# Optimization experiments

Measured on AMD Instinct MI355X. Metric: run time of the kernel, lower is better.

The kernel has to match this reference:

```python
import jax, jax.numpy as jnp
import numpy as np

N = 51200      # num nodes
E = 614400     # num edges
G = 256        # num graphs
T = 8          # num target capsules (GCNConv heads)
D = 128        # in_channels == out_channels
ROUTES = 3     # num_routes
BN_EPS = 1e-5


def squash(s):
    # s: (..., D). v = |s|^2/(1+|s|^2) * s/|s|
    s2 = jnp.sum(s * s, axis=-1, keepdims=True)
    return (s2 / (1.0 + s2)) * s * jax.lax.rsqrt(s2 + 1e-16)


def setup_inputs() -> dict:
    key = jax.random.key(0)
    k0, k1, k2, k3 = jax.random.split(key, 4)
    x = jax.random.normal(k0, (N, D), dtype=jnp.float32)
    edge_index = jax.random.randint(k1, (2, E), 0, N, dtype=jnp.int32)
    batch = jnp.sort(jax.random.randint(k2, (N,), 0, G, dtype=jnp.int32))
    edge_weight = jnp.ones((E,), dtype=jnp.float32)
    gamma = jnp.ones((D,), dtype=jnp.float32)
    beta = jnp.zeros((D,), dtype=jnp.float32)
    W = jax.random.normal(k3, (T, D, D), dtype=jnp.float32) * (1.0 / np.sqrt(D))
    bias = jnp.zeros((T, D), dtype=jnp.float32)
    return {"x": x, "edge_weight": edge_weight, "gamma": gamma, "beta": beta,
            "W": W, "bias": bias, "edge_index": edge_index, "batch": batch}


def reference(x, edge_weight, gamma, beta, W, bias, edge_index, batch):
    n = x.shape[0]
    row, col = edge_index[0], edge_index[1]

    # BatchNorm1d (training-mode batch stats)
    mu = jnp.mean(x, axis=0)
    var = jnp.var(x, axis=0)
    x = (x - mu) * jax.lax.rsqrt(var + BN_EPS) * gamma + beta

    # --- GCNConv per target capsule (PyG gcn_norm with self-loops) ---
    sl = jnp.arange(n, dtype=row.dtype)
    row_sl = jnp.concatenate([row, sl])
    col_sl = jnp.concatenate([col, sl])
    w_sl = jnp.concatenate([edge_weight, jnp.ones((n,), x.dtype)])
    deg = jax.ops.segment_sum(w_sl, col_sl, num_segments=n)
    dis = jnp.where(deg > 0, jax.lax.rsqrt(jnp.maximum(deg, 1e-12)), 0.0)
    norm = dis[row_sl] * w_sl * dis[col_sl]          # (E+N,)

    xW = jnp.einsum('nd,tdo->nto', x, W)             # (N, T, D)
    caps = []
    for t in range(T):  # small fixed loop over capsule heads keeps edge msgs at (E+N, D)
        msg = norm[:, None] * xW[row_sl, t]          # (E+N, D)
        caps.append(jax.ops.segment_sum(msg, col_sl, num_segments=n) + bias[t])
    u_hat = jnp.stack(caps, axis=1)                  # (N, T, D)

    # --- dynamic routing ---
    node_deg = jax.ops.segment_sum(edge_weight, row, num_segments=n)  # original edges, no self loops
    b = jnp.broadcast_to(node_deg[:, None, None], (n, T, 1))
    u_det = jax.lax.stop_gradient(u_hat)
    for _ in range(ROUTES - 1):
        c = jax.nn.softmax(b, axis=1)                               # (N, T, 1)
        s = jax.ops.segment_sum(c * u_det, batch, num_segments=G)   # (G, T, D)
        v = squash(s)[batch]                                        # (N, T, D)
        b = b + jnp.sum(u_det * v, axis=-1, keepdims=True)

    c = jax.nn.softmax(b, axis=1)
    s = jax.ops.segment_sum(c * u_hat, batch, num_segments=G)        # (G, T, D)
    cnt = jax.ops.segment_sum(jnp.ones((n,), x.dtype), batch, num_segments=G)
    x_mean = jax.ops.segment_sum(x, batch, num_segments=G) / jnp.maximum(cnt, 1.0)[:, None]
    s = s + x_mean[:, None, :]
    v = squash(s)
    # final_layer=True: per-capsule L2 norm -> (G, T)
    return jnp.sqrt(jnp.sum(v * v, axis=-1) + 1e-16)
```

## Files before the change

kernel.cpp:

```cpp
#include <hip/hip_runtime.h>
#include <hip/hip_bf16.h>
#include <math.h>

#define N_NODES 51200
#define N_EDGES 614400
#define N_GRAPHS 256
#define T_CAPS 8
#define D_DIM 128
#define BN_EPS 1e-5f
#define RCAP 256
#define NBUCK 200
#define BCAP 4096
#define EPB 1024
#define SBLK 600

typedef __attribute__((ext_vector_type(8))) __bf16 bf16x8;
typedef __attribute__((ext_vector_type(8))) unsigned short ushort8;
typedef __attribute__((ext_vector_type(4))) float f32x4;

__device__ inline f32x4 mfma16(uint4 a, uint4 b, f32x4 c) {
  return __builtin_amdgcn_mfma_f32_16x16x32_bf16(
      __builtin_bit_cast(bf16x8, a), __builtin_bit_cast(bf16x8, b), c, 0, 0, 0);
}
__device__ inline f32x4 mfma16v(uint4 a, ushort8 b, f32x4 c) {
  return __builtin_amdgcn_mfma_f32_16x16x32_bf16(
      __builtin_bit_cast(bf16x8, a), __builtin_bit_cast(bf16x8, b), c, 0, 0, 0);
}

__device__ inline float waveReduceSum(float v) {
#pragma unroll
  for (int off = 1; off < 64; off <<= 1) v += __shfl_xor(v, off, 64);
  return v;
}
__device__ inline float bf_lo(unsigned u) { return __uint_as_float(u << 16); }
__device__ inline float bf_hi(unsigned u) { return __uint_as_float(u & 0xffff0000u); }
__device__ inline unsigned bfbits(float f) {
  unsigned u = __float_as_uint(f);
  return (u + 0x7FFFu + ((u >> 16) & 1u)) >> 16;
}

__global__ void __launch_bounds__(256) prep(const int* __restrict__ batch,
                                            const float* __restrict__ W,
                                            int* __restrict__ start, int* __restrict__ bcur,
                                            unsigned* __restrict__ Wp,
                                            unsigned* __restrict__ WTp,
                                            float* __restrict__ rawzero) {
  int i = blockIdx.x * 256 + threadIdx.x;
  if (i < NBUCK) bcur[i] = 0;
  for (int j = i; j < 2 * N_GRAPHS * D_DIM; j += N_NODES) rawzero[j] = 0.f;
  int bn = batch[i];
  if (i == 0) {
    for (int g = 0; g <= bn; g++) start[g] = 0;
  } else {
    int bp = batch[i - 1];
    for (int g = bp + 1; g <= bn; g++) start[g] = i;
  }
  if (i == N_NODES - 1)
    for (int g = bn + 1; g <= N_GRAPHS; g++) start[g] = N_NODES;
  for (int j = i; j < 65536; j += N_NODES) {
    int t = j >> 13, r = j & 8191;
    int k = r >> 7, o = r & 127;
    float a = W[(t << 14) + (k << 8) + o];
    float b = W[(t << 14) + (k << 8) + 128 + o];
    Wp[j] = bfbits(a) | (bfbits(b) << 16);
    float2 w2 = ((const float2*)W)[(t << 13) + (o << 6) + k];
    WTp[j] = bfbits(w2.x) | (bfbits(w2.y) << 16);
  }
}

__global__ void __launch_bounds__(256) scatter_x(
    const int* __restrict__ row, const int* __restrict__ col, const float* __restrict__ ew,
    int* __restrict__ bcur, uint2* __restrict__ ebuck, const float* __restrict__ x,
    const int* __restrict__ start, float* __restrict__ rawxsum, float* __restrict__ rawxsq) {
  int bid = blockIdx.x, tid = threadIdx.x;
  if (bid < SBLK) {
    __shared__ uint2 staged[EPB];
    __shared__ int hcnt[256], lbase[256], gbase[256], wpart[4];
    unsigned rx[4], ry[4];
    int bk[4], idx[4];
    int base4 = bid * 256 + tid;
    int4 c4 = ((const int4*)col)[base4];
    int4 r4 = ((const int4*)row)[base4];
    float4 w4 = ((const float4*)ew)[base4];
    rx[0] = ((unsigned)c4.x << 16) | (unsigned)r4.x; ry[0] = bfbits(w4.x); bk[0] = c4.x >> 8;
    rx[1] = ((unsigned)c4.y << 16) | (unsigned)r4.y; ry[1] = bfbits(w4.y); bk[1] = c4.y >> 8;
    rx[2] = ((unsigned)c4.z << 16) | (unsigned)r4.z; ry[2] = bfbits(w4.z); bk[2] = c4.z >> 8;
    rx[3] = ((unsigned)c4.w << 16) | (unsigned)r4.w; ry[3] = bfbits(w4.w); bk[3] = c4.w >> 8;
    hcnt[tid] = 0;
    __syncthreads();
#pragma unroll
    for (int k = 0; k < 4; k++) idx[k] = atomicAdd(&hcnt[bk[k]], 1);
    __syncthreads();
    int v = hcnt[tid];
    int lane = tid & 63, wid = tid >> 6;
    int s = v;
#pragma unroll
    for (int off = 1; off < 64; off <<= 1) {
      int t = __shfl_up(s, off, 64);
      if (lane >= off) s += t;
    }
    if (lane == 63) wpart[wid] = s;
    if (tid < NBUCK) gbase[tid] = atomicAdd(&bcur[tid], v);
    __syncthreads();
    int add = 0;
    for (int w2 = 0; w2 < wid; w2++) add += wpart[w2];
    lbase[tid] = s + add - v;
    __syncthreads();
#pragma unroll
    for (int k = 0; k < 4; k++) staged[lbase[bk[k]] + idx[k]] = make_uint2(rx[k], ry[k]);
    __syncthreads();
    for (int i = tid; i < EPB; i += 256) {
      uint2 r = staged[i];
      int b = r.x >> 24;
      int pos = gbase[b] + (i - lbase[b]);
      if (pos < BCAP) ebuck[b * BCAP + pos] = r;
    }
    return;
  }
  int b2 = bid - SBLK;
  int g = b2 >> 2, sub = b2 & 3;
  __shared__ float ls[8][128], ls2[8][128];
  int q = tid & 31, h = tid >> 5;
  int st = start[g], en = start[g + 1];
  const float4* x4 = (const float4*)x;
  float4 s = make_float4(0.f, 0.f, 0.f, 0.f), s2 = make_float4(0.f, 0.f, 0.f, 0.f);
  for (int n = st + sub * 8 + h; n < en; n += 32) {
    float4 v = x4[n * 32 + q];
    s.x += v.x; s.y += v.y; s.z += v.z; s.w += v.w;
    s2.x += v.x * v.x; s2.y += v.y * v.y; s2.z += v.z * v.z; s2.w += v.w * v.w;
  }
  *(float4*)&ls[h][4 * q] = s;
  *(float4*)&ls2[h][4 * q] = s2;
  __syncthreads();
  if (tid < 128) {
    float a = 0.f;
#pragma unroll
    for (int hh = 0; hh < 8; hh++) a += ls[hh][tid];
    atomicAdd(&rawxsum[g * D_DIM + tid], a);
  } else {
    int d = tid - 128;
    float a = 0.f;
#pragma unroll
    for (int hh = 0; hh < 8; hh++) a += ls2[hh][d];
    atomicAdd(&rawxsq[g * D_DIM + d], a);
  }
}

__global__ void __launch_bounds__(256) bn_fin(const float* __restrict__ rawxsum,
                                              const float* __restrict__ rawxsq,
                                              const float* __restrict__ gamma,
                                              const float* __restrict__ beta,
                                              float* __restrict__ scale,
                                              float* __restrict__ shift) {
  int d = blockIdx.x;
  int tid = threadIdx.x;
  __shared__ float ls[256], ls2[256];
  ls[tid] = rawxsum[tid * D_DIM + d];
  ls2[tid] = rawxsq[tid * D_DIM + d];
  __syncthreads();
  for (int off = 128; off; off >>= 1) {
    if (tid < off) {
      ls[tid] += ls[tid + off];
      ls2[tid] += ls2[tid + off];
    }
    __syncthreads();
  }
  if (tid == 0) {
    float mu = ls[0] * (1.0f / N_NODES);
    float var = ls2[0] * (1.0f / N_NODES) - mu * mu;
    float rstd = rsqrtf(var + BN_EPS);
    float sc = gamma[d] * rstd;
    scale[d] = sc;
    shift[d] = beta[d] - mu * sc;
  }
}

__global__ void __launch_bounds__(256) build(const uint2* __restrict__ ebuck,
                                             const int* __restrict__ bcur,
                                             unsigned* __restrict__ csr,
                                             int* __restrict__ nstart, int* __restrict__ ncnt,
                                             const float* __restrict__ x,
                                             const float* __restrict__ scale,
                                             const float* __restrict__ shift,
                                             float* __restrict__ dis,
                                             __hip_bfloat162* __restrict__ y) {
  int b = blockIdx.x, tid = threadIdx.x;
  __shared__ uint2 staged[BCAP];
  __shared__ unsigned outr[BCAP];
  __shared__ int hist[256], pref[256], cur[256], wpart[4];
  __shared__ float dis_l[256];
  int cnt = min(bcur[b], BCAP);
  for (int i = tid; i < cnt; i += 256) staged[i] = ebuck[b * BCAP + i];
  hist[tid] = 0;
  __syncthreads();
  for (int i = tid; i < cnt; i += 256) {
    int dl = (staged[i].x >> 16) & 255;
    atomicAdd(&hist[dl], 1);
  }
  __syncthreads();
  int v = hist[tid];
  int lane = tid & 63, wid = tid >> 6;
  int s = v;
#pragma unroll
  for (int off = 1; off < 64; off <<= 1) {
    int t = __shfl_up(s, off, 64);
    if (lane >= off) s += t;
  }
  if (lane == 63) wpart[wid] = s;
  __syncthreads();
  int add = 0;
  for (int w2 = 0; w2 < wid; w2++) add += wpart[w2];
  int p0 = s + add - v;
  pref[tid] = p0;
  cur[tid] = p0;
  __syncthreads();
  for (int i = tid; i < cnt; i += 256) {
    uint2 r = staged[i];
    int dl = (r.x >> 16) & 255;
    int p = atomicAdd(&cur[dl], 1);
    outr[p] = ((r.x & 0xFFFFu) << 16) | r.y;
  }
  __syncthreads();
  for (int i = tid; i < cnt; i += 256) csr[b * BCAP + i] = outr[i];
  int n = b * 256 + tid;
  int hc = hist[tid];
  nstart[n] = b * BCAP + p0;
  ncnt[n] = hc;
  float sw = 0.f;
  for (int j = p0; j < p0 + hc; j++) sw += bf_lo(outr[j]);
  float dv = sw + 1.0f;
  float dn = dv > 0.f ? rsqrtf(fmaxf(dv, 1e-12f)) : 0.f;
  dis[n] = dn;
  dis_l[tid] = dn;
  __syncthreads();
  const float4* x4 = (const float4*)x;
  const float4* sc4 = (const float4*)scale;
  const float4* sh4 = (const float4*)shift;
  uint2* y2 = (uint2*)y;
  for (int i = tid; i < 256 * 32; i += 256) {
    int nl = i >> 5, l = i & 31;
    float dnl = dis_l[nl];
    float4 scv = sc4[l], shv = sh4[l];
    float4 xv = x4[(b * 256 + nl) * 32 + l];
    unsigned u0 = bfbits(dnl * (xv.x * scv.x + shv.x)) |
                  (bfbits(dnl * (xv.y * scv.y + shv.y)) << 16);
    unsigned u1 = bfbits(dnl * (xv.z * scv.z + shv.z)) |
                  (bfbits(dnl * (xv.w * scv.w + shv.w)) << 16);
    y2[(b * 256 + nl) * 32 + l] = make_uint2(u0, u1);
  }
}

__global__ void __launch_bounds__(256) node_gather(const __hip_bfloat162* __restrict__ y,
                                                   const float* __restrict__ dis,
                                                   const int* __restrict__ nstart,
                                                   const int* __restrict__ ncnt,
                                                   const unsigned* __restrict__ csr,
                                                   __hip_bfloat162* __restrict__ agg) {
  int n = blockIdx.x * 4 + (threadIdx.x >> 6);
  int lane = threadIdx.x & 63;
  int st = nstart[n], c = ncnt[n];
  float2 a = __bfloat1622float2(y[n * 64 + lane]);
  int j = 0;
  for (; j + 4 <= c; j += 4) {
    unsigned r0 = csr[st + j], r1 = csr[st + j + 1], r2 = csr[st + j + 2],
             r3 = csr[st + j + 3];
    float2 v0 = __bfloat1622float2(y[(r0 >> 16) * 64 + lane]);
    float2 v1 = __bfloat1622float2(y[(r1 >> 16) * 64 + lane]);
    float2 v2 = __bfloat1622float2(y[(r2 >> 16) * 64 + lane]);
    float2 v3 = __bfloat1622float2(y[(r3 >> 16) * 64 + lane]);
    float w0 = bf_lo(r0), w1 = bf_lo(r1), w2 = bf_lo(r2), w3 = bf_lo(r3);
    a.x += w0 * v0.x + w1 * v1.x + w2 * v2.x + w3 * v3.x;
    a.y += w0 * v0.y + w1 * v1.y + w2 * v2.y + w3 * v3.y;
  }
  for (; j < c; j++) {
    unsigned r = csr[st + j];
    float2 v = __bfloat1622float2(y[(r >> 16) * 64 + lane]);
    float w = bf_lo(r);
    a.x += w * v.x;
    a.y += w * v.y;
  }
  float dn = dis[n];
  a.x *= dn;
  a.y *= dn;
  agg[n * 64 + lane] = __float22bfloat162_rn(a);
}

__global__ void __launch_bounds__(1024) routing_fused(
    const unsigned* __restrict__ agg_bf, const int* __restrict__ start,
    const unsigned* __restrict__ Wp, const unsigned* __restrict__ WTp,
    const float* __restrict__ bias, const float* __restrict__ rawxsum,
    const float* __restrict__ scale, const float* __restrict__ shift,
    float* __restrict__ out) {
  int g = blockIdx.x;
  int tid = threadIdx.x;
  int st = start[g], c = start[g + 1] - st;

  __shared__ unsigned ag_sh[RCAP * 68];
  __shared__ float dt_sh[384][T_CAPS];
  __shared__ float ac_sh[T_CAPS][D_DIM];
  __shared__ float s_sh[T_CAPS][D_DIM];
  __shared__ float wv_sh[T_CAPS][132];
  __shared__ unsigned wvpk[2][16][68];
  __shared__ unsigned short ctb[2][16][264];
  __shared__ float csum_sh[T_CAPS], bv_sh[T_CAPS], f_sh[T_CAPS], s2p[T_CAPS][2];
  __shared__ float csp_sh[32];

  float* scratch = &dt_sh[0][0];
  const uint4* aggb4 = (const uint4*)agg_bf;
  uint4* ag4 = (uint4*)ag_sh;

  for (int i = tid; i < T_CAPS * 132; i += 1024) (&wv_sh[0][0])[i] = 0.f;
  for (int i = tid; i < 2 * 16 * 68; i += 1024) (&wvpk[0][0][0])[i] = 0u;
  for (int i = tid; i < 2 * 16 * 264; i += 1024) (&ctb[0][0][0])[i] = 0;
  if (tid < T_CAPS) {
    bv_sh[tid] = 0.f;
    csum_sh[tid] = 0.125f * (float)c;
  }
  {
    int d2 = tid & 63, h = tid >> 6;
    float sx = 0.f, sy = 0.f;
    for (int n = st + h; n < st + c; n += 16) {
      unsigned u = agg_bf[n * 64 + d2];
      sx += bf_lo(u);
      sy += bf_hi(u);
    }
    scratch[h * 128 + d2 * 2] = sx;
    scratch[h * 128 + d2 * 2 + 1] = sy;
  }
  __syncthreads();
  if (tid < 128) {
    float s = 0.f;
#pragma unroll
    for (int h = 0; h < 16; h++) s += scratch[h * 128 + tid];
    s *= 0.125f;
#pragma unroll
    for (int t = 0; t < T_CAPS; t++) ac_sh[t][tid] = s;
  }
  __syncthreads();

  int tG = tid >> 7, oG = tid & 127;
  int lane = tid & 63, wv_ = tid >> 6;

  for (int iter = 0; iter < 3; iter++) {
    {
      const unsigned* Wpt = Wp + (tG << 13);
      float s = 0.f;
#pragma unroll 8
      for (int k = 0; k < 64; k++) {
        unsigned u = Wpt[(k << 7) + oG];
        s += ac_sh[tG][2 * k] * bf_lo(u) + ac_sh[tG][2 * k + 1] * bf_hi(u);
      }
      s += csum_sh[tG] * bias[(tG << 7) + oG];
      if (iter == 2) {
        float cf = (float)c;
        float ic = 1.0f / fmaxf(cf, 1.0f);
        s += (scale[oG] * rawxsum[g * D_DIM + oG] + cf * shift[oG]) * ic;
      }
      s_sh[tG][oG] = s;
      float p = waveReduceSum(s * s);
      if ((tid & 63) == 0) s2p[tG][(tid >> 6) & 1] = p;
    }
    __syncthreads();
    if (tid < T_CAPS) {
      float s2 = s2p[tid][0] + s2p[tid][1];
      float f = (s2 / (1.0f + s2)) * rsqrtf(s2 + 1e-16f);
      f_sh[tid] = f;
      if (iter == 2) out[g * T_CAPS + tid] = sqrtf(f * f * s2 + 1e-16f);
    }
    __syncthreads();
    if (iter == 2) return;
    {
      const unsigned* WTpt = WTp + (tG << 13);
      float s = 0.f;
#pragma unroll 8
      for (int k = 0; k < 64; k++) {
        unsigned u = WTpt[(k << 7) + oG];
        s += s_sh[tG][2 * k] * bf_lo(u) + s_sh[tG][2 * k + 1] * bf_hi(u);
      }
      wv_sh[tG][oG] += f_sh[tG] * s;
      float bp = bias[(tG << 7) + oG] * s_sh[tG][oG];
      bp = waveReduceSum(bp);
      if ((tid & 63) == 0) s2p[tG][(tid >> 6) & 1] = bp;
    }
    __syncthreads();
    if (tid < T_CAPS) bv_sh[tid] += f_sh[tid] * (s2p[tid][0] + s2p[tid][1]);
    __syncthreads();
    for (int i = tid; i < 512; i += 1024) {
      int t = i >> 6, kp = i & 63;
      float a = wv_sh[t][2 * kp], b = wv_sh[t][2 * kp + 1];
      unsigned ha = bfbits(a), hb = bfbits(b);
      wvpk[0][t][kp] = ha | (hb << 16);
      float ra = a - __uint_as_float(ha << 16), rb = b - __uint_as_float(hb << 16);
      wvpk[1][t][kp] = bfbits(ra) | (bfbits(rb) << 16);
    }
    if (tid < 1024) {
      (&ac_sh[0][0])[tid] = 0.f;
    }
    if (tid < T_CAPS) csum_sh[tid] = 0.f;
    __syncthreads();

    for (int cb = 0; cb < c; cb += RCAP) {
      int nv = min(RCAP, c - cb);
      int KR32 = (nv + 31) & ~31;
      int Mt = (nv + 15) >> 4;
      if (iter == 0 || c > RCAP) {
        for (int i = tid; i < nv * 16; i += 1024) {
          int r = i >> 4, k = i & 15;
          ag4[r * 17 + k] = aggb4[(size_t)(st + cb + r) * 16 + k];
        }
        for (int i = tid; i < (KR32 - nv) * 16; i += 1024) {
          int r = nv + (i >> 4), k = i & 15;
          ag4[r * 17 + k] = make_uint4(0, 0, 0, 0);
        }
        __syncthreads();
      }
      if (wv_ < Mt) {
        int q = lane >> 4, tc = lane & 15;
        int r = wv_ * 16 + tc;
        const uint4* arow = ag4 + r * 17;
        f32x4 C = {0.f, 0.f, 0.f, 0.f};
#pragma unroll
        for (int ks = 0; ks < 4; ks++) {
          uint4 A = arow[ks * 4 + q];
          uint4 Bh = *(const uint4*)&wvpk[0][tc][ks * 16 + 4 * q];
          uint4 Bl = *(const uint4*)&wvpk[1][tc][ks * 16 + 4 * q];
          C = mfma16(A, Bh, C);
          C = mfma16(A, Bl, C);
        }
        if (tc < T_CAPS) {
          float bvv = bv_sh[tc];
#pragma unroll
          for (int i2 = 0; i2 < 4; i2++) dt_sh[wv_ * 16 + 4 * q + i2][tc] = C[i2] + bvv;
        }
      }
      __syncthreads();
      if (tid < nv) {
        float l[8];
#pragma unroll
        for (int t = 0; t < 8; t++) l[t] = dt_sh[tid][t];
        float m = l[0];
#pragma unroll
        for (int t = 1; t < 8; t++) m = fmaxf(m, l[t]);
        float z = 0.f;
#pragma unroll
        for (int t = 0; t < 8; t++) {
          l[t] = __expf(l[t] - m);
          z += l[t];
        }
        float iz = 1.0f / z;
#pragma unroll
        for (int t = 0; t < 8; t++) {
          float cv = l[t] * iz;
          dt_sh[tid][t] = cv;
          unsigned hb = bfbits(cv);
          ctb[0][t][tid] = (unsigned short)hb;
          ctb[1][t][tid] = (unsigned short)bfbits(cv - __uint_as_float(hb << 16));
        }
      }
      if (c > RCAP) {
        int tail = KR32 - nv;
        for (int i = tid; i < 16 * tail; i += 1024) {
          int hh = i & 1, t = (i >> 1) & 7, n2 = nv + (i >> 4);
          ctb[hh][t][n2] = 0;
        }
      }
      __syncthreads();
      {
        int tA = tid >> 7, idx = tid & 127;
        float p = 0.f;
        for (int n = idx; n < nv; n += 128) p += dt_sh[n][tA];
        p = waveReduceSum(p);
        if (lane == 0) csp_sh[wv_] = p;
      }
      __syncthreads();
      if (tid < T_CAPS) csum_sh[tid] += csp_sh[2 * tid] + csp_sh[2 * tid + 1];
      {
        int nt = wv_ & 7, kh = wv_ >> 3;
        int tc = lane & 15, q = lane >> 4;
        f32x4 C = {0.f, 0.f, 0.f, 0.f};
        const unsigned short* agh = (const unsigned short*)ag_sh;
        int KS = KR32 >> 5;
        for (int ks = kh; ks < KS; ks += 2) {
          uint4 Ah = *(const uint4*)&ctb[0][tc][ks * 32 + 8 * q];
          uint4 Al = *(const uint4*)&ctb[1][tc][ks * 32 + 8 * q];
          int nb = ks * 32 + 8 * q, dcol = nt * 16 + tc;
          ushort8 B;
#pragma unroll
          for (int j = 0; j < 8; j++) B[j] = agh[(nb + j) * 136 + dcol];
          C = mfma16v(Ah, B, C);
          C = mfma16v(Al, B, C);
        }
        if (kh == 1) *(f32x4*)&scratch[(nt * 64 + lane) * 4] = C;
        __syncthreads();
        if (kh == 0) {
          f32x4 o4 = *(const f32x4*)&scratch[(nt * 64 + lane) * 4];
          C.x += o4.x;
          C.y += o4.y;
          C.z += o4.z;
          C.w += o4.w;
#pragma unroll
          for (int i2 = 0; i2 < 4; i2++) {
            int tt = 4 * q + i2;
            if (tt < T_CAPS) ac_sh[tt][nt * 16 + tc] += C[i2];
          }
        }
      }
      __syncthreads();
    }
  }
}

extern "C" void kernel_launch(void* const* d_in, const int* in_sizes, int n_in, void* d_out,
                              int out_size, void* d_ws, size_t ws_size, hipStream_t stream) {
  const float* x = (const float*)d_in[0];
  const float* ew = (const float*)d_in[1];
  const float* gamma = (const float*)d_in[2];
  const float* beta = (const float*)d_in[3];
  const float* W = (const float*)d_in[4];
  const float* bias = (const float*)d_in[5];
  const int* eidx = (const int*)d_in[6];
  const int* batch = (const int*)d_in[7];
  float* out = (float*)d_out;
  float* w = (float*)d_ws;

  const int* row = eidx;
  const int* col = eidx + N_EDGES;

  int* bcur = (int*)w;
  int* start = bcur + 256;
  float* scale = (float*)(start + 260);
  float* shift = scale + 128;
  float* dis = shift + 128;
  float* rawxsum = dis + N_NODES;
  float* rawxsq = rawxsum + N_GRAPHS * D_DIM;
  unsigned* Wp = (unsigned*)(rawxsq + N_GRAPHS * D_DIM);
  unsigned* WTp = Wp + 65536;
  int* nstart = (int*)(WTp + 65536);
  int* ncnt = nstart + N_NODES;
  uint2* ebuck = (uint2*)(ncnt + N_NODES);
  unsigned* csr = (unsigned*)(ebuck + (size_t)NBUCK * BCAP);
  __hip_bfloat162* y = (__hip_bfloat162*)(csr + (size_t)NBUCK * BCAP);
  unsigned* agg_bf = (unsigned*)(y + (size_t)N_NODES * 64);

  prep<<<N_NODES / 256, 256, 0, stream>>>(batch, W, start, bcur, Wp, WTp, rawxsum);
  scatter_x<<<SBLK + 4 * N_GRAPHS, 256, 0, stream>>>(row, col, ew, bcur, ebuck, x, start,
                                                     rawxsum, rawxsq);
  bn_fin<<<D_DIM, 256, 0, stream>>>(rawxsum, rawxsq, gamma, beta, scale, shift);
  build<<<NBUCK, 256, 0, stream>>>(ebuck, bcur, csr, nstart, ncnt, x, scale, shift, dis, y);
  node_gather<<<N_NODES / 4, 256, 0, stream>>>(y, dis, nstart, ncnt, csr,
                                               (__hip_bfloat162*)agg_bf);
  routing_fused<<<N_GRAPHS, 1024, 0, stream>>>(agg_bf, start, Wp, WTp, bias, rawxsum, scale,
                                               shift, out);
}
```

Measured before the change: 187.3 us.

## Use MFMA for per-graph capsule matvecs in routing kernel

The per-iteration matrix-vector products with W and W^T in the routing kernel move from scalar FMA loops over packed bf16 weights to MFMA 16x16x32 instructions. Weights are pre-swizzled into fragment layout in the prep kernel. Activations are split into bf16 hi/lo pairs held in two rows of the A operand, which keeps extra precision. The cost is extra syncs and a mostly-zero A tile (only 2 of 16 rows are used), in exchange for fewer scalar instructions and coalesced uint4 weight loads.

```diff
diff --git a/kernel.cpp b/kernel.cpp
--- a/kernel.cpp
+++ b/kernel.cpp
@@ -42,8 +42,8 @@
 __global__ void __launch_bounds__(256) prep(const int* __restrict__ batch,
                                             const float* __restrict__ W,
                                             int* __restrict__ start, int* __restrict__ bcur,
-                                            unsigned* __restrict__ Wp,
-                                            unsigned* __restrict__ WTp,
+                                            unsigned* __restrict__ Wfrag,
+                                            unsigned* __restrict__ WTfrag,
                                             float* __restrict__ rawzero) {
   int i = blockIdx.x * 256 + threadIdx.x;
   if (i < NBUCK) bcur[i] = 0;
@@ -57,14 +57,16 @@
   }
   if (i == N_NODES - 1)
     for (int g = bn + 1; g <= N_GRAPHS; g++) start[g] = N_NODES;
-  for (int j = i; j < 65536; j += N_NODES) {
-    int t = j >> 13, r = j & 8191;
-    int k = r >> 7, o = r & 127;
-    float a = W[(t << 14) + (k << 8) + o];
-    float b = W[(t << 14) + (k << 8) + 128 + o];
-    Wp[j] = bfbits(a) | (bfbits(b) << 16);
-    float2 w2 = ((const float2*)W)[(t << 13) + (o << 6) + k];
-    WTp[j] = bfbits(w2.x) | (bfbits(w2.y) << 16);
+  for (int dd = i; dd < 65536; dd += N_NODES) {
+    int jj = dd & 3, lane = (dd >> 2) & 63, ks = (dd >> 8) & 3;
+    int nt = (dd >> 10) & 7, t = dd >> 13;
+    int k = ks * 32 + ((lane >> 4) << 3) + 2 * jj;
+    int n = nt * 16 + (lane & 15);
+    float a = W[(t << 14) + (k << 7) + n];
+    float b = W[(t << 14) + ((k + 1) << 7) + n];
+    Wfrag[dd] = bfbits(a) | (bfbits(b) << 16);
+    float2 w2 = ((const float2*)W)[((t << 14) + (n << 7) + k) >> 1];
+    WTfrag[dd] = bfbits(w2.x) | (bfbits(w2.y) << 16);
   }
 }
 
@@ -287,7 +289,7 @@
 
 __global__ void __launch_bounds__(1024) routing_fused(
     const unsigned* __restrict__ agg_bf, const int* __restrict__ start,
-    const unsigned* __restrict__ Wp, const unsigned* __restrict__ WTp,
+    const unsigned* __restrict__ Wfrag, const unsigned* __restrict__ WTfrag,
     const float* __restrict__ bias, const float* __restrict__ rawxsum,
     const float* __restrict__ scale, const float* __restrict__ shift,
     float* __restrict__ out) {
@@ -302,6 +304,8 @@
   __shared__ float wv_sh[T_CAPS][132];
   __shared__ unsigned wvpk[2][16][68];
   __shared__ unsigned short ctb[2][16][264];
+  __shared__ unsigned acpk[T_CAPS][2][64];
+  __shared__ unsigned spk[T_CAPS][2][64];
   __shared__ float csum_sh[T_CAPS], bv_sh[T_CAPS], f_sh[T_CAPS], s2p[T_CAPS][2];
   __shared__ float csp_sh[32];
 
@@ -343,14 +347,42 @@
 
   for (int iter = 0; iter < 3; iter++) {
     {
-      const unsigned* Wpt = Wp + (tG << 13);
-      float s = 0.f;
-#pragma unroll 8
-      for (int k = 0; k < 64; k++) {
-        unsigned u = Wpt[(k << 7) + oG];
-        s += ac_sh[tG][2 * k] * bf_lo(u) + ac_sh[tG][2 * k + 1] * bf_hi(u);
-      }
-      s += csum_sh[tG] * bias[(tG << 7) + oG];
+      int t = tid >> 7, m = (tid >> 6) & 1, kp = tid & 63;
+      float a = ac_sh[t][2 * kp], b = ac_sh[t][2 * kp + 1];
+      unsigned ha = bfbits(a), hb = bfbits(b);
+      if (m == 0)
+        acpk[t][0][kp] = ha | (hb << 16);
+      else
+        acpk[t][1][kp] = bfbits(a - __uint_as_float(ha << 16)) |
+                         (bfbits(b - __uint_as_float(hb << 16)) << 16);
+    }
+    __syncthreads();
+    {
+      int t = wv_ & 7, oh = wv_ >> 3;
+      int m = lane & 15, q = lane >> 4;
+      const uint4* Wf = (const uint4*)Wfrag;
+      f32x4 C0 = {0.f, 0.f, 0.f, 0.f}, C1 = C0, C2 = C0, C3 = C0;
+#pragma unroll
+      for (int ks = 0; ks < 4; ks++) {
+        uint4 A = (m < 2) ? *(const uint4*)&acpk[t][m][ks * 16 + q * 4]
+                          : make_uint4(0, 0, 0, 0);
+        int base = ((t * 8 + oh * 4) * 4 + ks) * 64 + lane;
+        C0 = mfma16(A, Wf[base], C0);
+        C1 = mfma16(A, Wf[base + 256], C1);
+        C2 = mfma16(A, Wf[base + 512], C2);
+        C3 = mfma16(A, Wf[base + 768], C3);
+      }
+      if (q == 0) {
+        int o0 = oh * 64 + m;
+        s_sh[t][o0] = C0[0] + C0[1];
+        s_sh[t][o0 + 16] = C1[0] + C1[1];
+        s_sh[t][o0 + 32] = C2[0] + C2[1];
+        s_sh[t][o0 + 48] = C3[0] + C3[1];
+      }
+    }
+    __syncthreads();
+    {
+      float s = s_sh[tG][oG] + csum_sh[tG] * bias[(tG << 7) + oG];
       if (iter == 2) {
         float cf = (float)c;
         float ic = 1.0f / fmaxf(cf, 1.0f);
@@ -361,6 +393,16 @@
       if ((tid & 63) == 0) s2p[tG][(tid >> 6) & 1] = p;
     }
     __syncthreads();
+    {
+      int t = tid >> 7, m = (tid >> 6) & 1, kp = tid & 63;
+      float a = s_sh[t][2 * kp], b = s_sh[t][2 * kp + 1];
+      unsigned ha = bfbits(a), hb = bfbits(b);
+      if (m == 0)
+        spk[t][0][kp] = ha | (hb << 16);
+      else
+        spk[t][1][kp] = bfbits(a - __uint_as_float(ha << 16)) |
+                        (bfbits(b - __uint_as_float(hb << 16)) << 16);
+    }
     if (tid < T_CAPS) {
       float s2 = s2p[tid][0] + s2p[tid][1];
       float f = (s2 / (1.0f + s2)) * rsqrtf(s2 + 1e-16f);
@@ -370,14 +412,31 @@
     __syncthreads();
     if (iter == 2) return;
     {
-      const unsigned* WTpt = WTp + (tG << 13);
-      float s = 0.f;
-#pragma unroll 8
-      for (int k = 0; k < 64; k++) {
-        unsigned u = WTpt[(k << 7) + oG];
-        s += s_sh[tG][2 * k] * bf_lo(u) + s_sh[tG][2 * k + 1] * bf_hi(u);
-      }
-      wv_sh[tG][oG] += f_sh[tG] * s;
+      int t = wv_ & 7, oh = wv_ >> 3;
+      int m = lane & 15, q = lane >> 4;
+      const uint4* Wf = (const uint4*)WTfrag;
+      f32x4 C0 = {0.f, 0.f, 0.f, 0.f}, C1 = C0, C2 = C0, C3 = C0;
+#pragma unroll
+      for (int ks = 0; ks < 4; ks++) {
+        uint4 A = (m < 2) ? *(const uint4*)&spk[t][m][ks * 16 + q * 4]
+                          : make_uint4(0, 0, 0, 0);
+        int base = ((t * 8 + oh * 4) * 4 + ks) * 64 + lane;
+        C0 = mfma16(A, Wf[base], C0);
+        C1 = mfma16(A, Wf[base + 256], C1);
+        C2 = mfma16(A, Wf[base + 512], C2);
+        C3 = mfma16(A, Wf[base + 768], C3);
+      }
+      if (q == 0) {
+        int o0 = oh * 64 + m;
+        scratch[t * 128 + o0] = C0[0] + C0[1];
+        scratch[t * 128 + o0 + 16] = C1[0] + C1[1];
+        scratch[t * 128 + o0 + 32] = C2[0] + C2[1];
+        scratch[t * 128 + o0 + 48] = C3[0] + C3[1];
+      }
+    }
+    __syncthreads();
+    {
+      wv_sh[tG][oG] += f_sh[tG] * scratch[tG * 128 + oG];
       float bp = bias[(tG << 7) + oG] * s_sh[tG][oG];
       bp = waveReduceSum(bp);
       if ((tid & 63) == 0) s2p[tG][(tid >> 6) & 1] = bp;
@@ -533,22 +592,22 @@
   float* dis = shift + 128;
   float* rawxsum = dis + N_NODES;
   float* rawxsq = rawxsum + N_GRAPHS * D_DIM;
-  unsigned* Wp = (unsigned*)(rawxsq + N_GRAPHS * D_DIM);
-  unsigned* WTp = Wp + 65536;
-  int* nstart = (int*)(WTp + 65536);
+  unsigned* Wfrag = (unsigned*)(rawxsq + N_GRAPHS * D_DIM);
+  unsigned* WTfrag = Wfrag + 65536;
+  int* nstart = (int*)(WTfrag + 65536);
   int* ncnt = nstart + N_NODES;
   uint2* ebuck = (uint2*)(ncnt + N_NODES);
   unsigned* csr = (unsigned*)(ebuck + (size_t)NBUCK * BCAP);
   __hip_bfloat162* y = (__hip_bfloat162*)(csr + (size_t)NBUCK * BCAP);
   unsigned* agg_bf = (unsigned*)(y + (size_t)N_NODES * 64);
 
-  prep<<<N_NODES / 256, 256, 0, stream>>>(batch, W, start, bcur, Wp, WTp, rawxsum);
+  prep<<<N_NODES / 256, 256, 0, stream>>>(batch, W, start, bcur, Wfrag, WTfrag, rawxsum);
   scatter_x<<<SBLK + 4 * N_GRAPHS, 256, 0, stream>>>(row, col, ew, bcur, ebuck, x, start,
                                                      rawxsum, rawxsq);
   bn_fin<<<D_DIM, 256, 0, stream>>>(rawxsum, rawxsq, gamma, beta, scale, shift);
   build<<<NBUCK, 256, 0, stream>>>(ebuck, bcur, csr, nstart, ncnt, x, scale, shift, dis, y);
   node_gather<<<N_NODES / 4, 256, 0, stream>>>(y, dis, nstart, ncnt, csr,
                                                (__hip_bfloat162*)agg_bf);
-  routing_fused<<<N_GRAPHS, 1024, 0, stream>>>(agg_bf, start, Wp, WTp, bias, rawxsum, scale,
-                                               shift, out);
-}
+  routing_fused<<<N_GRAPHS, 1024, 0, stream>>>(agg_bf, start, Wfrag, WTfrag, bias, rawxsum,
+                                               scale, shift, out);
+}
```

Measured after the change: 227.0 us. 1.21x slower.
